# Performance work log

Measured on AMD Instinct MI355X. Metric: run time of the kernel, lower is better.

The kernel has to match this reference:

```python
import math
import jax, jax.numpy as jnp
import numpy as np

B, LA, LB, H = 16, 1024, 1024, 512
NEG = -10000000.0


def setup_inputs() -> dict:
    key = jax.random.key(0)
    k1, k2, k3, k4 = jax.random.split(key, 4)
    a = jax.random.normal(k1, (B, LA, H), dtype=jnp.float32)
    b = jax.random.normal(k2, (B, LB, H), dtype=jnp.float32)
    mask_a = jax.random.randint(k3, (B, LA, 1), 0, 2, dtype=jnp.int32)
    mask_b = jax.random.randint(k4, (B, LB, 1), 0, 2, dtype=jnp.int32)
    temperature = jnp.asarray(1.0 / math.sqrt(H), dtype=jnp.float32)
    return {"a": a, "b": b, "mask_a": mask_a, "mask_b": mask_b, "temperature": temperature}


def reference(a, b, mask_a, mask_b, temperature):
    # attn[b,i,j] = <a_i, b_j> * temperature  -> [B, LA, LB]
    attn = jnp.einsum("bid,bjd->bij", a, b) * temperature
    # pairwise validity mask: outer product of per-token masks
    mask = jnp.einsum("bik,bjk->bij", mask_a.astype(jnp.float32), mask_b.astype(jnp.float32)) > 0
    attn = jnp.where(mask, attn, NEG)
    attn_a = jax.nn.softmax(attn, axis=1)  # softmax over a-tokens
    attn_b = jax.nn.softmax(attn, axis=2)  # softmax over b-tokens
    feature_b = jnp.einsum("bij,bid->bjd", attn_a, a)  # [B, LB, H]
    feature_a = jnp.einsum("bij,bjd->bid", attn_b, b)  # [B, LA, H]
    return (feature_a, feature_b)
```

## Files before the change

kernel.cpp:

```cpp
#include <hip/hip_runtime.h>
#include <hip/hip_bf16.h>

#define NB_ 16
#define LA_ 1024
#define LB_ 1024
#define H_  512

typedef __attribute__((ext_vector_type(8))) short short8;
typedef __attribute__((ext_vector_type(4))) float f32x4;

using bf16 = __hip_bfloat16;

__device__ __forceinline__ float bf2f(unsigned short u) {
    union { unsigned int i; float f; } c; c.i = ((unsigned)u) << 16; return c.f;
}
__device__ __forceinline__ unsigned short f2bf(float f) {
    bf16 h = __float2bfloat16(f);
    return *(unsigned short*)&h;
}

__device__ __forceinline__ void load_lds16(const void* g, void* l) {
    __builtin_amdgcn_global_load_lds(
        (const __attribute__((address_space(1))) void*)g,
        (__attribute__((address_space(3))) void*)l, 16, 0, 0);
}

__device__ __forceinline__ void gemm_core256(
    const unsigned short* __restrict__ A, const unsigned short* __restrict__ B,
    int lda, int ldb, int K,
    unsigned short* lds, f32x4 acc[8][4])
{
    const int t = threadIdx.x;
    const int w = t >> 6, lane = t & 63;
    const int wr = w >> 2, wc = w & 3;
    const int lm = lane & 15, q = lane >> 4;

    int aoff[8], boff[4];
#pragma unroll
    for (int f = 0; f < 8; f++) {
        const int ra = wr * 128 + f * 16 + lm;
        aoff[f] = ra * 128 + ((q ^ (ra & 7)) << 4);
    }
#pragma unroll
    for (int f = 0; f < 4; f++) {
        const int rb = wc * 64 + f * 16 + lm;
        boff[f] = rb * 128 + ((q ^ (rb & 7)) << 4);
    }

    const int rstep = w * 8 + (lane >> 3);
    const int sc = (lane & 7) ^ (lane >> 3);
    const unsigned short* gA = A + (size_t)rstep * lda + sc * 8;
    const unsigned short* gB = B + (size_t)rstep * ldb + sc * 8;
    char* lA = (char*)lds + w * 1024;
    char* lB = (char*)lds + 65536 + w * 1024;
    const int NT = K >> 6;

#pragma unroll
    for (int s = 0; s < 4; s++) {
        load_lds16(gA + (size_t)s * 64 * lda, lA + s * 8192);
        load_lds16(gB + (size_t)s * 64 * ldb, lB + s * 8192);
    }
    __syncthreads();

    int db = 0;
    for (int kt = 0; kt < NT; ++kt) {
        const char* bA = (const char*)lds + db * 32768;
        const char* bB = (const char*)lds + 65536 + db * 32768;
        const int nxt = (db ^ 1) * 32768;
        short8 av[4][2];
#pragma unroll
        for (int p = 0; p < 4; ++p) {
            const int pm = p >> 1, pn = p & 1;
            if (p == 0 && kt + 1 < NT) {
                const size_t ko = (size_t)(kt + 1) * 64;
#pragma unroll
                for (int s = 0; s < 4; s++) {
                    load_lds16(gA + ko + (size_t)s * 64 * lda, lA + nxt + s * 8192);
                    load_lds16(gB + ko + (size_t)s * 64 * ldb, lB + nxt + s * 8192);
                }
            }
            if (pn == 0) {
#pragma unroll
                for (int f = 0; f < 4; f++)
#pragma unroll
                    for (int kk = 0; kk < 2; kk++)
                        av[f][kk] = *(const short8*)(bA + (aoff[pm * 4 + f] ^ (kk << 6)));
            }
            short8 bv[2][2];
#pragma unroll
            for (int f = 0; f < 2; f++)
#pragma unroll
                for (int kk = 0; kk < 2; kk++)
                    bv[f][kk] = *(const short8*)(bB + (boff[pn * 2 + f] ^ (kk << 6)));
            __builtin_amdgcn_s_barrier();
            __builtin_amdgcn_s_setprio(1);
#pragma unroll
            for (int kk = 0; kk < 2; kk++)
#pragma unroll
                for (int f = 0; f < 2; f++)
#pragma unroll
                    for (int m = 0; m < 4; m++)
                        acc[pm * 4 + m][pn * 2 + f] =
                            __builtin_amdgcn_mfma_f32_16x16x32_bf16(
                                av[m][kk], bv[f][kk],
                                acc[pm * 4 + m][pn * 2 + f], 0, 0, 0);
            __builtin_amdgcn_s_setprio(0);
            if (p < 3) __builtin_amdgcn_s_barrier();
        }
        __syncthreads();
        db ^= 1;
    }
}

__global__ __launch_bounds__(512, 2) void k_gemm_attn(
    const unsigned short* __restrict__ a_bf, const unsigned short* __restrict__ b_bf,
    const int* __restrict__ mask_a, const int* __restrict__ mask_b,
    const float* __restrict__ temp_p,
    unsigned short* __restrict__ E, unsigned short* __restrict__ ET,
    float* __restrict__ l_row, float* __restrict__ l_col)
{
    __shared__ unsigned short lds[65536];

    const int g = blockIdx.x;
    const int batch = g & 15;
    const int qq = g >> 4;
    const int i0 = (qq >> 2) * 256, j0 = (qq & 3) * 256;

    const unsigned short* A = a_bf + (size_t)batch * LA_ * H_ + (size_t)i0 * H_;
    const unsigned short* B = b_bf + (size_t)batch * LB_ * H_ + (size_t)j0 * H_;
    f32x4 acc[8][4];
#pragma unroll
    for (int x = 0; x < 8; x++)
#pragma unroll
        for (int y = 0; y < 4; y++) acc[x][y] = 0;

    gemm_core256(A, B, H_, H_, H_, lds, acc);

    const float temp = temp_p[0];
    const int t = threadIdx.x, w = t >> 6, lane = t & 63;
    const int wr = w >> 2, wc = w & 3, lm = lane & 15, q = lane >> 4;
    const int* map = mask_a + batch * LA_;
    const int* mbp = mask_b + batch * LB_;
    unsigned short* Ep  = E  + (size_t)batch * LA_ * LB_;
    unsigned short* ETp = ET + (size_t)batch * LB_ * LA_;
    float* lrp = l_row + batch * LA_;
    float* lcp = l_col + batch * LB_;

    int mb4[4];
#pragma unroll
    for (int fn = 0; fn < 4; fn++) mb4[fn] = mbp[j0 + wc * 64 + fn * 16 + lm];

#pragma unroll
    for (int fm = 0; fm < 8; fm++) {
        const int ilb = wr * 128 + fm * 16 + q * 4;
        int ma[4];
#pragma unroll
        for (int r = 0; r < 4; r++) ma[r] = map[i0 + ilb + r];
#pragma unroll
        for (int fn = 0; fn < 4; fn++) {
            const int jl = wc * 64 + fn * 16 + lm;
            ushort4 pk;
            unsigned short* pp = (unsigned short*)&pk;
#pragma unroll
            for (int r = 0; r < 4; r++) {
                const float e = (ma[r] && mb4[fn]) ? __expf(acc[fm][fn][r] * temp) : 0.0f;
                acc[fm][fn][r] = e;
                pp[r] = f2bf(e);
                const int il = ilb + r;
                lds[il * 256 + ((((jl >> 3) ^ ((il >> 1) & 15)) << 3) | (jl & 7))] = pp[r];
            }
            *(ushort4*)(ETp + (size_t)(j0 + jl) * LA_ + i0 + ilb) = pk;
        }
    }

#pragma unroll
    for (int fm = 0; fm < 8; fm++)
#pragma unroll
        for (int r = 0; r < 4; r++) {
            float s = acc[fm][0][r] + acc[fm][1][r] + acc[fm][2][r] + acc[fm][3][r];
            s += __shfl_xor(s, 1, 16); s += __shfl_xor(s, 2, 16);
            s += __shfl_xor(s, 4, 16); s += __shfl_xor(s, 8, 16);
            if (lm == 0) atomicAdd(&lrp[i0 + wr * 128 + fm * 16 + q * 4 + r], s);
        }
#pragma unroll
    for (int fn = 0; fn < 4; fn++) {
        float s = 0.0f;
#pragma unroll
        for (int fm = 0; fm < 8; fm++)
#pragma unroll
            for (int r = 0; r < 4; r++) s += acc[fm][fn][r];
        s += __shfl_xor(s, 16, 64); s += __shfl_xor(s, 32, 64);
        if (lane < 16) atomicAdd(&lcp[j0 + wc * 64 + fn * 16 + lm], s);
    }

    __syncthreads();
#pragma unroll
    for (int rep = 0; rep < 16; rep++) {
        const int il = (t >> 5) + rep * 16;
        const int c = t & 31;
        const int phys = c ^ ((il >> 1) & 15);
        short8 v = *(const short8*)(lds + il * 256 + phys * 8);
        *(short8*)(Ep + (size_t)(i0 + il) * LB_ + j0 + c * 8) = v;
    }
}

__global__ __launch_bounds__(512, 2) void k_gemm_feat(
    const unsigned short* __restrict__ E, const unsigned short* __restrict__ ET,
    const unsigned short* __restrict__ aT, const unsigned short* __restrict__ bT,
    const int* __restrict__ mask_a, const int* __restrict__ mask_b,
    const int* __restrict__ nA, const int* __restrict__ nB,
    const float* __restrict__ l_row, const float* __restrict__ l_col,
    const float* __restrict__ mean_a, const float* __restrict__ mean_b,
    float* __restrict__ out)
{
    __shared__ unsigned short lds[65536];

    const int g = blockIdx.x;
    const int zc = g & 31;
    const int qq = g >> 5;
    const int n0 = (qq & 1) * 256, m0 = (qq >> 1) * 256;

    const int batch = zc & 15;
    const bool isA = zc < 16;
    const unsigned short* Amat = (isA ? E : ET) + (size_t)batch * 1024 * 1024;
    const unsigned short* Bm   = (isA ? bT : aT) + (size_t)batch * H_ * 1024;
    const int* mp   = (isA ? mask_a : mask_b) + batch * 1024;
    const int nn    = (isA ? nB : nA)[batch];
    const float* sp = (isA ? l_row : l_col) + batch * 1024;
    const float* mv = (isA ? mean_b : mean_a) + batch * H_;
    float* op = out + (isA ? (size_t)0 : (size_t)NB_ * LA_ * H_) + (size_t)batch * 1024 * H_;

    f32x4 acc[8][4];
#pragma unroll
    for (int x = 0; x < 8; x++)
#pragma unroll
        for (int y = 0; y < 4; y++) acc[x][y] = 0;

    gemm_core256(Amat + (size_t)m0 * 1024, Bm + (size_t)n0 * 1024,
                 1024, 1024, 1024, lds, acc);

    const int t = threadIdx.x, w = t >> 6, lane = t & 63;
    const int wr = w >> 2, wc = w & 3, lm = lane & 15, q = lane >> 4;

    float mval[4];
#pragma unroll
    for (int fn = 0; fn < 4; fn++) mval[fn] = mv[n0 + wc * 64 + fn * 16 + lm];

#pragma unroll
    for (int fm = 0; fm < 8; fm++) {
        const int ib = m0 + wr * 128 + fm * 16 + q * 4;
#pragma unroll
        for (int r = 0; r < 4; r++) {
            const int i = ib + r;
            const bool valid = (mp[i] != 0) && (nn > 0);
            const float inv = valid ? 1.0f / sp[i] : 0.0f;
#pragma unroll
            for (int fn = 0; fn < 4; fn++) {
                const int d = n0 + wc * 64 + fn * 16 + lm;
                op[(size_t)i * H_ + d] = valid ? acc[fm][fn][r] * inv : mval[fn];
            }
        }
    }
}

__global__ __launch_bounds__(256) void k_prep(
    const float* __restrict__ a, const float* __restrict__ b,
    unsigned short* __restrict__ aN, unsigned short* __restrict__ bN,
    unsigned short* __restrict__ aT, unsigned short* __restrict__ bT,
    float* __restrict__ mean_a, float* __restrict__ mean_b)
{
    __shared__ unsigned short lds[64][68];
    __shared__ float smean[64];
    const int z = blockIdx.z;
    const int batch = z & 15, sel = z >> 4;
    const float* src = sel ? b : a;
    unsigned short* np = (sel ? bN : aN) + (size_t)batch * 1024 * H_;
    unsigned short* tp = (sel ? bT : aT) + (size_t)batch * H_ * 1024;
    float* mdst = (sel ? mean_b : mean_a) + batch * H_;
    const float* sp = src + (size_t)batch * 1024 * H_;

    const int d0 = blockIdx.x * 64, i0 = blockIdx.y * 64;
    const int t = threadIdx.x;
    if (t < 64) smean[t] = 0.0f;
    const int c4 = (t & 15) * 4;
#pragma unroll
    for (int it = 0; it < 4; it++) {
        const int r = (t >> 4) + it * 16;
        float4 v = *(const float4*)(sp + (size_t)(i0 + r) * H_ + d0 + c4);
        ushort4 u = make_ushort4(f2bf(v.x), f2bf(v.y), f2bf(v.z), f2bf(v.w));
        *(ushort4*)(np + (size_t)(i0 + r) * H_ + d0 + c4) = u;
        *(ushort4*)&lds[r][c4] = u;
    }
    __syncthreads();
#pragma unroll
    for (int it = 0; it < 4; it++) {
        const int dd = (t >> 4) + it * 16;
        const int i4 = (t & 15) * 4;
        ushort4 u = make_ushort4(lds[i4][dd], lds[i4 + 1][dd], lds[i4 + 2][dd], lds[i4 + 3][dd]);
        *(ushort4*)(tp + (size_t)(d0 + dd) * 1024 + i0 + i4) = u;
        atomicAdd(&smean[dd], bf2f(u.x) + bf2f(u.y) + bf2f(u.z) + bf2f(u.w));
    }
    __syncthreads();
    if (t < 64) atomicAdd(&mdst[d0 + t], smean[t] * (1.0f / 1024.0f));
}

__global__ __launch_bounds__(256) void k_init(
    float* __restrict__ accum_zero,
    const int* __restrict__ mask_a, const int* __restrict__ mask_b,
    int* __restrict__ nA, int* __restrict__ nB)
{
    const int g = blockIdx.x, t = threadIdx.x;
    if (g < 48) {
        *(float4*)(accum_zero + (size_t)(g * 256 + t) * 4) = make_float4(0, 0, 0, 0);
        return;
    }
    const int sel = g - 48;
    const int batch = sel & 15, which = sel >> 4;
    const int* m = (which ? mask_b : mask_a) + batch * 1024;
    int s = m[t] + m[t + 256] + m[t + 512] + m[t + 768];
    __shared__ int red[256];
    red[t] = s;
    __syncthreads();
    for (int off = 128; off; off >>= 1) {
        if (t < off) red[t] += red[t + off];
        __syncthreads();
    }
    if (t == 0) (which ? nB : nA)[batch] = red[0];
}

extern "C" void kernel_launch(void* const* d_in, const int* in_sizes, int n_in,
                              void* d_out, int out_size, void* d_ws, size_t ws_size,
                              hipStream_t stream)
{
    const float* a      = (const float*)d_in[0];
    const float* b      = (const float*)d_in[1];
    const int*   mask_a = (const int*)d_in[2];
    const int*   mask_b = (const int*)d_in[3];
    const float* temp   = (const float*)d_in[4];
    float* out = (float*)d_out;

    char* ws = (char*)d_ws;
    size_t off = 0;
    unsigned short* E    = (unsigned short*)(ws + off); off += (size_t)NB_ * LA_ * LB_ * 2;
    unsigned short* ET   = (unsigned short*)(ws + off); off += (size_t)NB_ * LB_ * LA_ * 2;
    unsigned short* a_bf = (unsigned short*)(ws + off); off += (size_t)NB_ * LA_ * H_ * 2;
    unsigned short* b_bf = (unsigned short*)(ws + off); off += (size_t)NB_ * LB_ * H_ * 2;
    unsigned short* aT   = (unsigned short*)(ws + off); off += (size_t)NB_ * H_ * LA_ * 2;
    unsigned short* bT   = (unsigned short*)(ws + off); off += (size_t)NB_ * H_ * LB_ * 2;
    float* l_row  = (float*)(ws + off); off += (size_t)NB_ * LA_ * 4;
    float* l_col  = (float*)(ws + off); off += (size_t)NB_ * LB_ * 4;
    float* mean_a = (float*)(ws + off); off += (size_t)NB_ * H_ * 4;
    float* mean_b = (float*)(ws + off); off += (size_t)NB_ * H_ * 4;
    int*   nA     = (int*)(ws + off); off += 64;
    int*   nB     = (int*)(ws + off); off += 64;

    k_init<<<dim3(80), 256, 0, stream>>>(l_row, mask_a, mask_b, nA, nB);

    k_prep<<<dim3(H_ / 64, 1024 / 64, 32), 256, 0, stream>>>(
        a, b, a_bf, b_bf, aT, bT, mean_a, mean_b);

    k_gemm_attn<<<dim3(256), 512, 0, stream>>>(
        a_bf, b_bf, mask_a, mask_b, temp, E, ET, l_row, l_col);

    k_gemm_feat<<<dim3(256), 512, 0, stream>>>(
        E, ET, aT, bT, mask_a, mask_b, nA, nB, l_row, l_col, mean_a, mean_b, out);
}
```

Measured before the change: 220.2 us.

## Stagger next-tile LDS prefetch across MFMA phases with fine-grained vmcnt waits

Rewrites the GEMM main loop so that global-to-LDS loads for the next K tile are spread over the four MFMA phases instead of all being issued at the start. Full __syncthreads are replaced with explicit s_waitcnt vmcnt counts plus s_barrier. The loop is unrolled by two with templated buffer indices, so LDS offsets become compile-time constants. The goal is smoother memory issue and less stall at tile boundaries. In exchange, correctness now depends on precise vmcnt accounting and on NT being even.

```diff
diff --git a/kernel.cpp b/kernel.cpp
--- a/kernel.cpp
+++ b/kernel.cpp
@@ -23,6 +23,70 @@
     __builtin_amdgcn_global_load_lds(
         (const __attribute__((address_space(1))) void*)g,
         (__attribute__((address_space(3))) void*)l, 16, 0, 0);
+}
+
+template<int DB, int MODE>
+__device__ __forceinline__ void gemm_tile256(
+    const unsigned short* __restrict__ gA, const unsigned short* __restrict__ gB,
+    int lda, int ldb, size_t ko,
+    unsigned short* lds, char* lA, char* lB,
+    const int* aoff, const int* boff, f32x4 acc[8][4])
+{
+    const char* bA = (const char*)lds + DB * 32768;
+    const char* bB = (const char*)lds + 65536 + DB * 32768;
+    const int nxt = (DB ^ 1) * 32768;
+    short8 av[4][2];
+#pragma unroll
+    for (int p = 0; p < 4; ++p) {
+        const int pm = p >> 1, pn = p & 1;
+        if (pn == 0) {
+#pragma unroll
+            for (int f = 0; f < 4; f++)
+#pragma unroll
+                for (int kk = 0; kk < 2; kk++)
+                    av[f][kk] = *(const short8*)(bA + (aoff[pm * 4 + f] ^ (kk << 6)));
+        }
+        short8 bv[2][2];
+#pragma unroll
+        for (int f = 0; f < 2; f++)
+#pragma unroll
+            for (int kk = 0; kk < 2; kk++)
+                bv[f][kk] = *(const short8*)(bB + (boff[pn * 2 + f] ^ (kk << 6)));
+        if (MODE == 0) {
+            if (p == 0) {
+                load_lds16(gB + ko,                       lB + nxt);
+                load_lds16(gB + ko + (size_t)64 * ldb,    lB + nxt + 8192);
+            } else if (p == 1) {
+                load_lds16(gB + ko + (size_t)128 * ldb,   lB + nxt + 16384);
+                load_lds16(gB + ko + (size_t)192 * ldb,   lB + nxt + 24576);
+            } else if (p == 2) {
+                load_lds16(gA + ko,                       lA + nxt);
+                load_lds16(gA + ko + (size_t)128 * lda,   lA + nxt + 16384);
+            } else {
+                load_lds16(gA + ko + (size_t)64 * lda,    lA + nxt + 8192);
+                load_lds16(gA + ko + (size_t)192 * lda,   lA + nxt + 24576);
+            }
+        }
+        __builtin_amdgcn_s_barrier();
+        __builtin_amdgcn_s_setprio(1);
+#pragma unroll
+        for (int kk = 0; kk < 2; kk++)
+#pragma unroll
+            for (int f = 0; f < 2; f++)
+#pragma unroll
+                for (int m = 0; m < 4; m++)
+                    acc[pm * 4 + m][pn * 2 + f] =
+                        __builtin_amdgcn_mfma_f32_16x16x32_bf16(
+                            av[m][kk], bv[f][kk],
+                            acc[pm * 4 + m][pn * 2 + f], 0, 0, 0);
+        __builtin_amdgcn_s_setprio(0);
+        if (p == 1) {
+            if (MODE == 0) asm volatile("s_waitcnt vmcnt(4)" ::: "memory");
+            else           asm volatile("s_waitcnt vmcnt(0)" ::: "memory");
+        }
+        if (p == 3 && MODE == 0) asm volatile("s_waitcnt vmcnt(2)" ::: "memory");
+        if (p < 3 || MODE == 0) __builtin_amdgcn_s_barrier();
+    }
 }
 
 __device__ __forceinline__ void gemm_core256(
@@ -55,61 +119,28 @@
     char* lB = (char*)lds + 65536 + w * 1024;
     const int NT = K >> 6;
 
-#pragma unroll
-    for (int s = 0; s < 4; s++) {
-        load_lds16(gA + (size_t)s * 64 * lda, lA + s * 8192);
-        load_lds16(gB + (size_t)s * 64 * ldb, lB + s * 8192);
-    }
-    __syncthreads();
-
-    int db = 0;
-    for (int kt = 0; kt < NT; ++kt) {
-        const char* bA = (const char*)lds + db * 32768;
-        const char* bB = (const char*)lds + 65536 + db * 32768;
-        const int nxt = (db ^ 1) * 32768;
-        short8 av[4][2];
-#pragma unroll
-        for (int p = 0; p < 4; ++p) {
-            const int pm = p >> 1, pn = p & 1;
-            if (p == 0 && kt + 1 < NT) {
-                const size_t ko = (size_t)(kt + 1) * 64;
-#pragma unroll
-                for (int s = 0; s < 4; s++) {
-                    load_lds16(gA + ko + (size_t)s * 64 * lda, lA + nxt + s * 8192);
-                    load_lds16(gB + ko + (size_t)s * 64 * ldb, lB + nxt + s * 8192);
-                }
-            }
-            if (pn == 0) {
-#pragma unroll
-                for (int f = 0; f < 4; f++)
-#pragma unroll
-                    for (int kk = 0; kk < 2; kk++)
-                        av[f][kk] = *(const short8*)(bA + (aoff[pm * 4 + f] ^ (kk << 6)));
-            }
-            short8 bv[2][2];
-#pragma unroll
-            for (int f = 0; f < 2; f++)
-#pragma unroll
-                for (int kk = 0; kk < 2; kk++)
-                    bv[f][kk] = *(const short8*)(bB + (boff[pn * 2 + f] ^ (kk << 6)));
-            __builtin_amdgcn_s_barrier();
-            __builtin_amdgcn_s_setprio(1);
-#pragma unroll
-            for (int kk = 0; kk < 2; kk++)
-#pragma unroll
-                for (int f = 0; f < 2; f++)
-#pragma unroll
-                    for (int m = 0; m < 4; m++)
-                        acc[pm * 4 + m][pn * 2 + f] =
-                            __builtin_amdgcn_mfma_f32_16x16x32_bf16(
-                                av[m][kk], bv[f][kk],
-                                acc[pm * 4 + m][pn * 2 + f], 0, 0, 0);
-            __builtin_amdgcn_s_setprio(0);
-            if (p < 3) __builtin_amdgcn_s_barrier();
-        }
-        __syncthreads();
-        db ^= 1;
-    }
+    load_lds16(gB,                       lB);
+    load_lds16(gB + (size_t)64 * ldb,    lB + 8192);
+    load_lds16(gB + (size_t)128 * ldb,   lB + 16384);
+    load_lds16(gB + (size_t)192 * ldb,   lB + 24576);
+    load_lds16(gA,                       lA);
+    load_lds16(gA + (size_t)128 * lda,   lA + 16384);
+    load_lds16(gA + (size_t)64 * lda,    lA + 8192);
+    load_lds16(gA + (size_t)192 * lda,   lA + 24576);
+    asm volatile("s_waitcnt vmcnt(2)" ::: "memory");
+    __builtin_amdgcn_s_barrier();
+
+    int kt = 0;
+    for (; kt + 2 < NT; kt += 2) {
+        gemm_tile256<0, 0>(gA, gB, lda, ldb, (size_t)(kt + 1) * 64,
+                           lds, lA, lB, aoff, boff, acc);
+        gemm_tile256<1, 0>(gA, gB, lda, ldb, (size_t)(kt + 2) * 64,
+                           lds, lA, lB, aoff, boff, acc);
+    }
+    gemm_tile256<0, 0>(gA, gB, lda, ldb, (size_t)(NT - 1) * 64,
+                       lds, lA, lB, aoff, boff, acc);
+    gemm_tile256<1, 1>(gA, gB, lda, ldb, 0, lds, lA, lB, aoff, boff, acc);
+    __syncthreads();
 }
 
 __global__ __launch_bounds__(512, 2) void k_gemm_attn(
```

Measured after the change: 215.3 us. 1.02x faster.
